# Kernel optimization log

Hardware: AMD Instinct MI355X
Metric: run time of the kernel (lower is better)

## Reference

```python
import jax, jax.numpy as jnp
import numpy as np

NEG_NUM = -10000.0
PRUNE_L, PRUNE_R = -3, 3  # prune_range


def setup_inputs() -> dict:
    key = jax.random.key(0)
    ks = jax.random.split(key, 8)
    B, L, D_CTX, D_Q, H = 32, 2048, 512, 1024, 256
    s = 0.02
    query = jax.random.normal(ks[0], (B, D_Q), jnp.float32)
    ctx = jax.random.normal(ks[1], (B, L, D_CTX), jnp.float32)
    # previous kappa (attention centre) spread over the source positions
    kappa_prev = jax.random.uniform(ks[2], (B, 1), jnp.float32) * L
    Wq = jax.random.normal(ks[3], (D_Q, H), jnp.float32) * s
    bq = jnp.zeros((H,), jnp.float32)
    Ws = jax.random.normal(ks[4], (H, 3), jnp.float32) * s
    # bias init: alpha_bias=0, beta_bias=-1, kappa_bias=-1
    bs = jnp.array([0.0, -1.0, -1.0], jnp.float32)
    W1 = jax.random.normal(ks[5], (D_CTX + D_Q, H), jnp.float32) * s
    b1 = jnp.zeros((H,), jnp.float32)
    W2 = jax.random.normal(ks[6], (H, 1), jnp.float32) * s
    b2 = jnp.zeros((1,), jnp.float32)
    return dict(query=query, ctx=ctx, kappa_prev=kappa_prev, Wq=Wq, bq=bq,
                Ws=Ws, bs=bs, W1=W1, b1=b1, W2=W2, b2=b2)


def reference(query, ctx, kappa_prev, Wq, bq, Ws, bs, W1, b1, W2, b2):
    B, L, D_CTX = ctx.shape
    # stat projection: alpha/beta/kappa (n_mixtures = 1)
    h = jnp.tanh(query @ Wq + bq)                       # [B, H]
    stat = h @ Ws + bs                                  # [B, 3]
    alpha = jnp.exp(stat[:, 0:1])                       # [B, 1]
    beta = jnp.exp(stat[:, 1:2])                        # [B, 1]
    kappa = jnp.exp(stat[:, 2:3]) + kappa_prev          # monotonic: [B, 1]

    pos = jnp.arange(L, dtype=jnp.float32)              # [L]
    diff = pos[None, :] - kappa                         # [B, L]
    prior = alpha * jnp.exp(-beta * diff * diff)        # [B, L]

    # local prune window around round(kappa) (mask built on detached kappa)
    center = jnp.round(jax.lax.stop_gradient(kappa))    # [B, 1]
    mask = (pos[None, :] >= center + PRUNE_L) & (pos[None, :] <= center + PRUNE_R)
    prior = jnp.where(mask, prior, 0.0)                 # [B, L]

    # MLP likelihood scorer over (ctx, query)
    q_exp = jnp.broadcast_to(query[:, None, :], (B, L, query.shape[1]))
    comb = jnp.concatenate([ctx, q_exp], axis=-1)       # [B, L, D_CTX+D_Q]
    score = (jnp.tanh(comb @ W1 + b1) @ W2 + b2)[..., 0]  # [B, L]
    score = jnp.where(mask, score, NEG_NUM)
    likelihood = jnp.exp(score)                         # [B, L]

    posterior = jnp.where(mask, likelihood * prior, 0.0)  # [B, L]
    p_ctx = posterior / jnp.sum(posterior, axis=-1, keepdims=True)  # normalize_post
    expected_ctx = jnp.einsum('bl,bld->bd', p_ctx, ctx)  # [B, D_CTX]
    return expected_ctx, p_ctx
```

## Files before the change

kernel.cpp:

```cpp
#include <hip/hip_runtime.h>
#include <cmath>

constexpr int B     = 32;
constexpr int L     = 2048;
constexpr int D_CTX = 512;
constexpr int D_Q   = 1024;
constexpr int H     = 256;
constexpr int PRUNE_L = -3;
constexpr int PRUNE_R = 3;
constexpr int W = PRUNE_R - PRUNE_L + 1;
constexpr int KC = 16;

__global__ __launch_bounds__(256) void partial_kernel(
    const float* __restrict__ query,
    const float* __restrict__ Wq,
    const float* __restrict__ W1,
    float* __restrict__ partQ,
    float* __restrict__ part1)
{
    const int kc = blockIdx.x;
    const int b  = blockIdx.y;
    const int j  = threadIdx.x;
    const int k0 = kc * (D_Q / KC);

    __shared__ float q_sh[D_Q / KC];
    if (j < D_Q / KC) q_sh[j] = query[b * D_Q + k0 + j];
    __syncthreads();

    const float* WqR = Wq + (size_t)k0 * H + j;
    const float* W1R = W1 + ((size_t)D_CTX + k0) * H + j;
    float accQ = 0.f, acc1 = 0.f;
#pragma unroll 16
    for (int k = 0; k < D_Q / KC; ++k) {
        const float qk = q_sh[k];
        accQ += qk * WqR[(size_t)k * H];
        acc1 += qk * W1R[(size_t)k * H];
    }
    partQ[((size_t)b * KC + kc) * H + j] = accQ;
    part1[((size_t)b * KC + kc) * H + j] = acc1;
}

__global__ __launch_bounds__(256) void stats_kernel(
    const float* __restrict__ kappa_prev,
    const float* __restrict__ bq,
    const float* __restrict__ Ws,
    const float* __restrict__ bs,
    const float* __restrict__ b1,
    const float* __restrict__ partQ,
    const float* __restrict__ part1,
    float* __restrict__ stats,
    float* __restrict__ qpre)
{
    const int b = blockIdx.x;
    const int j = threadIdx.x;

    float sq = 0.f, s1 = 0.f;
#pragma unroll
    for (int kc = 0; kc < KC; ++kc) {
        sq += partQ[((size_t)b * KC + kc) * H + j];
        s1 += part1[((size_t)b * KC + kc) * H + j];
    }
    __shared__ float h_sh[H];
    h_sh[j] = tanhf(sq + bq[j]);
    qpre[(size_t)b * H + j] = s1 + b1[j];
    __syncthreads();

    if (j < 64) {
        float s0 = 0.f, s1r = 0.f, s2 = 0.f;
#pragma unroll
        for (int i = 0; i < 4; ++i) {
            const int   jj = j + 64 * i;
            const float hv = h_sh[jj];
            s0  += hv * Ws[jj * 3 + 0];
            s1r += hv * Ws[jj * 3 + 1];
            s2  += hv * Ws[jj * 3 + 2];
        }
        for (int off = 32; off > 0; off >>= 1) {
            s0  += __shfl_down(s0, off);
            s1r += __shfl_down(s1r, off);
            s2  += __shfl_down(s2, off);
        }
        if (j == 0) {
            const float alpha = expf(s0 + bs[0]);
            const float beta  = expf(s1r + bs[1]);
            const float kappa = expf(s2 + bs[2]) + kappa_prev[b];
            stats[b * 4 + 0] = alpha;
            stats[b * 4 + 1] = beta;
            stats[b * 4 + 2] = kappa;
            stats[b * 4 + 3] = rintf(kappa);
        }
    }
}

__global__ __launch_bounds__(512) void score_kernel(
    const float* __restrict__ ctx,
    const float* __restrict__ W1,
    const float* __restrict__ W2,
    const float* __restrict__ b2,
    const float* __restrict__ stats,
    const float* __restrict__ qpre,
    float* __restrict__ post)
{
    const int t   = blockIdx.x;
    const int b   = blockIdx.y;
    const int tid = threadIdx.x;
    const int jg  = tid & 63;
    const int kc  = tid >> 6;

    const float alpha  = stats[b * 4 + 0];
    const float beta   = stats[b * 4 + 1];
    const float kappa  = stats[b * 4 + 2];
    const int   center = (int)stats[b * 4 + 3];
    const int   l      = center + PRUNE_L + t;

    if (l < 0 || l >= L) {
        if (tid == 0) post[b * W + t] = 0.0f;
        return;
    }

    __shared__ float  c_sh[D_CTX];
    __shared__ float4 part[8][64];
    __shared__ float  red[H];

    const float4* ctx4 = (const float4*)(ctx + ((size_t)b * L + (size_t)l) * D_CTX);
    if (tid < D_CTX / 4) ((float4*)c_sh)[tid] = ctx4[tid];
    __syncthreads();

    const float4* Wv = (const float4*)W1;
    float4 acc = make_float4(0.f, 0.f, 0.f, 0.f);
    const int k0 = kc * 64;
#pragma unroll 8
    for (int k = k0; k < k0 + 64; ++k) {
        const float  ck = c_sh[k];
        const float4 w  = Wv[k * 64 + jg];
        acc.x += ck * w.x; acc.y += ck * w.y;
        acc.z += ck * w.z; acc.w += ck * w.w;
    }
    part[kc][jg] = acc;
    __syncthreads();
    for (int s = 4; s > 0; s >>= 1) {
        if (kc < s) {
            float4 a = part[kc][jg], c = part[kc + s][jg];
            a.x += c.x; a.y += c.y; a.z += c.z; a.w += c.w;
            part[kc][jg] = a;
        }
        __syncthreads();
    }
    if (tid < H) {
        const float pre = ((const float*)part)[tid] + qpre[(size_t)b * H + tid];
        red[tid] = tanhf(pre) * W2[tid];
    }
    __syncthreads();
    for (int s = H / 2; s > 0; s >>= 1) {
        if (tid < s) red[tid] += red[tid + s];
        __syncthreads();
    }
    if (tid == 0) {
        const float score = red[0] + b2[0];
        const float diff  = (float)l - kappa;
        post[b * W + t] = expf(score) * alpha * expf(-beta * diff * diff);
    }
}

__global__ __launch_bounds__(256) void combine_kernel(
    const float* __restrict__ ctx,
    const float* __restrict__ stats,
    const float* __restrict__ post,
    float* __restrict__ out_e,
    float* __restrict__ out_p)
{
    const int b = blockIdx.x;
    const int j = threadIdx.x;

    __shared__ float p_sh[W];
    __shared__ int   l_sh[W];
    if (j == 0) {
        const int center = (int)stats[b * 4 + 3];
        float sum = 0.0f;
        for (int t = 0; t < W; ++t) sum += post[b * W + t];
        const float inv = 1.0f / sum;
        for (int t = 0; t < W; ++t) {
            p_sh[t] = post[b * W + t] * inv;
            l_sh[t] = center + PRUNE_L + t;
        }
    }
    __syncthreads();

    float4* prow = (float4*)(out_p + (size_t)b * L);
    const float4 z = make_float4(0.f, 0.f, 0.f, 0.f);
    prow[j]       = z;
    prow[j + 256] = z;
    __syncthreads();
    if (j < W) {
        const int l = l_sh[j];
        if (l >= 0 && l < L) out_p[(size_t)b * L + l] = p_sh[j];
    }

    if (j < D_CTX / 4) {
        float4 acc = make_float4(0.f, 0.f, 0.f, 0.f);
#pragma unroll
        for (int t = 0; t < W; ++t) {
            const int l = l_sh[t];
            if (l >= 0 && l < L) {
                const float4 c = ((const float4*)(ctx + ((size_t)b * L + (size_t)l) * D_CTX))[j];
                const float  p = p_sh[t];
                acc.x += p * c.x; acc.y += p * c.y;
                acc.z += p * c.z; acc.w += p * c.w;
            }
        }
        ((float4*)(out_e + (size_t)b * D_CTX))[j] = acc;
    }
}

extern "C" void kernel_launch(void* const* d_in, const int* in_sizes, int n_in,
                              void* d_out, int out_size, void* d_ws, size_t ws_size,
                              hipStream_t stream) {
    const float* query      = (const float*)d_in[0];
    const float* ctx        = (const float*)d_in[1];
    const float* kappa_prev = (const float*)d_in[2];
    const float* Wq         = (const float*)d_in[3];
    const float* bq         = (const float*)d_in[4];
    const float* Ws         = (const float*)d_in[5];
    const float* bs         = (const float*)d_in[6];
    const float* W1         = (const float*)d_in[7];
    const float* b1         = (const float*)d_in[8];
    const float* W2         = (const float*)d_in[9];
    const float* b2         = (const float*)d_in[10];

    float* out   = (float*)d_out;
    float* out_e = out;
    float* out_p = out + B * D_CTX;

    float* stats = (float*)d_ws;
    float* qpre  = stats + B * 4;
    float* post  = qpre + B * H;
    float* partQ = post + B * W + 8;
    float* part1 = partQ + B * KC * H;

    partial_kernel<<<dim3(KC, B), 256, 0, stream>>>(query, Wq, W1, partQ, part1);
    stats_kernel<<<B, 256, 0, stream>>>(kappa_prev, bq, Ws, bs, b1,
                                        partQ, part1, stats, qpre);
    score_kernel<<<dim3(W, B), 512, 0, stream>>>(ctx, W1, W2, b2, stats, qpre, post);
    combine_kernel<<<B, 256, 0, stream>>>(ctx, stats, post, out_e, out_p);
}
```

Baseline: 198.5 us.

## Fuse stats into score kernel, prefetch W1 rows, vectorize partial GEMV, split combine

Removes the separate stats kernel: each score block now recomputes the partial-sum reduction, tanh, the Ws projection and alpha/beta/kappa itself. Before those values are ready, it prefetches the first 16 W1 rows into registers to hide their load latency. The partial kernel now uses float4 weight loads with a 4-way k split reduced in shared memory, and the score tail uses a warp shuffle reduction instead of the shared-memory tree. Combine is spread over 8 blocks per batch row for zeroing out_p. The cost is redundant stats work across the 7 window blocks per batch and higher register pressure from the prefetched weights.

New measurement: 199.3 us. No clear change (+0.4%).

```diff
diff --git a/kernel.cpp b/kernel.cpp
--- a/kernel.cpp
+++ b/kernel.cpp
@@ -18,99 +18,121 @@
     float* __restrict__ partQ,
     float* __restrict__ part1)
 {
-    const int kc = blockIdx.x;
-    const int b  = blockIdx.y;
-    const int j  = threadIdx.x;
-    const int k0 = kc * (D_Q / KC);
-
-    __shared__ float q_sh[D_Q / KC];
-    if (j < D_Q / KC) q_sh[j] = query[b * D_Q + k0 + j];
-    __syncthreads();
-
-    const float* WqR = Wq + (size_t)k0 * H + j;
-    const float* W1R = W1 + ((size_t)D_CTX + k0) * H + j;
-    float accQ = 0.f, acc1 = 0.f;
-#pragma unroll 16
-    for (int k = 0; k < D_Q / KC; ++k) {
-        const float qk = q_sh[k];
-        accQ += qk * WqR[(size_t)k * H];
-        acc1 += qk * W1R[(size_t)k * H];
-    }
-    partQ[((size_t)b * KC + kc) * H + j] = accQ;
-    part1[((size_t)b * KC + kc) * H + j] = acc1;
-}
-
-__global__ __launch_bounds__(256) void stats_kernel(
+    const int kc  = blockIdx.x;
+    const int b   = blockIdx.y;
+    const int tid = threadIdx.x;
+    const int jg  = tid & 63;
+    const int sub = tid >> 6;
+
+    __shared__ float q_sh[64];
+    if (tid < 64) q_sh[tid] = query[b * D_Q + kc * 64 + tid];
+    __syncthreads();
+
+    const float4* WqV = (const float4*)Wq;
+    const float4* W1V = (const float4*)(W1 + (size_t)D_CTX * H);
+    float4 aQ = make_float4(0.f, 0.f, 0.f, 0.f);
+    float4 a1 = make_float4(0.f, 0.f, 0.f, 0.f);
+    const int kbase = kc * 64 + sub * 16;
+#pragma unroll
+    for (int kk = 0; kk < 16; ++kk) {
+        const int    k  = kbase + kk;
+        const float  qk = q_sh[sub * 16 + kk];
+        const float4 wq = WqV[(size_t)k * 64 + jg];
+        const float4 w1 = W1V[(size_t)k * 64 + jg];
+        aQ.x += qk * wq.x; aQ.y += qk * wq.y; aQ.z += qk * wq.z; aQ.w += qk * wq.w;
+        a1.x += qk * w1.x; a1.y += qk * w1.y; a1.z += qk * w1.z; a1.w += qk * w1.w;
+    }
+
+    __shared__ float4 pq[4][64];
+    __shared__ float4 p1[4][64];
+    pq[sub][jg] = aQ;
+    p1[sub][jg] = a1;
+    __syncthreads();
+
+    const float* pqf = (const float*)pq;
+    const float* p1f = (const float*)p1;
+    const float sQ = pqf[tid] + pqf[256 + tid] + pqf[512 + tid] + pqf[768 + tid];
+    const float s1 = p1f[tid] + p1f[256 + tid] + p1f[512 + tid] + p1f[768 + tid];
+    partQ[((size_t)b * KC + kc) * H + tid] = sQ;
+    part1[((size_t)b * KC + kc) * H + tid] = s1;
+}
+
+__global__ __launch_bounds__(512) void score_kernel(
+    const float* __restrict__ ctx,
     const float* __restrict__ kappa_prev,
     const float* __restrict__ bq,
     const float* __restrict__ Ws,
     const float* __restrict__ bs,
     const float* __restrict__ b1,
+    const float* __restrict__ W1,
+    const float* __restrict__ W2,
+    const float* __restrict__ b2,
     const float* __restrict__ partQ,
     const float* __restrict__ part1,
     float* __restrict__ stats,
-    float* __restrict__ qpre)
-{
-    const int b = blockIdx.x;
-    const int j = threadIdx.x;
-
-    float sq = 0.f, s1 = 0.f;
-#pragma unroll
-    for (int kc = 0; kc < KC; ++kc) {
-        sq += partQ[((size_t)b * KC + kc) * H + j];
-        s1 += part1[((size_t)b * KC + kc) * H + j];
-    }
-    __shared__ float h_sh[H];
-    h_sh[j] = tanhf(sq + bq[j]);
-    qpre[(size_t)b * H + j] = s1 + b1[j];
-    __syncthreads();
-
-    if (j < 64) {
-        float s0 = 0.f, s1r = 0.f, s2 = 0.f;
-#pragma unroll
-        for (int i = 0; i < 4; ++i) {
-            const int   jj = j + 64 * i;
-            const float hv = h_sh[jj];
-            s0  += hv * Ws[jj * 3 + 0];
-            s1r += hv * Ws[jj * 3 + 1];
-            s2  += hv * Ws[jj * 3 + 2];
-        }
-        for (int off = 32; off > 0; off >>= 1) {
-            s0  += __shfl_down(s0, off);
-            s1r += __shfl_down(s1r, off);
-            s2  += __shfl_down(s2, off);
-        }
-        if (j == 0) {
-            const float alpha = expf(s0 + bs[0]);
-            const float beta  = expf(s1r + bs[1]);
-            const float kappa = expf(s2 + bs[2]) + kappa_prev[b];
-            stats[b * 4 + 0] = alpha;
-            stats[b * 4 + 1] = beta;
-            stats[b * 4 + 2] = kappa;
-            stats[b * 4 + 3] = rintf(kappa);
-        }
-    }
-}
-
-__global__ __launch_bounds__(512) void score_kernel(
-    const float* __restrict__ ctx,
-    const float* __restrict__ W1,
-    const float* __restrict__ W2,
-    const float* __restrict__ b2,
-    const float* __restrict__ stats,
-    const float* __restrict__ qpre,
     float* __restrict__ post)
 {
     const int t   = blockIdx.x;
     const int b   = blockIdx.y;
     const int tid = threadIdx.x;
     const int jg  = tid & 63;
-    const int kc  = tid >> 6;
-
-    const float alpha  = stats[b * 4 + 0];
-    const float beta   = stats[b * 4 + 1];
-    const float kappa  = stats[b * 4 + 2];
-    const int   center = (int)stats[b * 4 + 3];
+    const int kc8 = tid >> 6;
+    const int k0  = kc8 * 64;
+
+    const float4* Wv = (const float4*)W1;
+    float4 wpre[16];
+#pragma unroll
+    for (int i = 0; i < 16; ++i) wpre[i] = Wv[(size_t)(k0 + i) * 64 + jg];
+
+    __shared__ float qpre_sh[H];
+    __shared__ float h_sh[H];
+    __shared__ float s_sh[4];
+    if (tid < H) {
+        float s = 0.f;
+#pragma unroll
+        for (int kc = 0; kc < KC; ++kc) s += part1[((size_t)b * KC + kc) * H + tid];
+        qpre_sh[tid] = s + b1[tid];
+    } else {
+        const int j = tid - H;
+        float s = 0.f;
+#pragma unroll
+        for (int kc = 0; kc < KC; ++kc) s += partQ[((size_t)b * KC + kc) * H + j];
+        h_sh[j] = tanhf(s + bq[j]);
+    }
+    __syncthreads();
+
+    if (tid < 64) {
+        float s0 = 0.f, s1 = 0.f, s2 = 0.f;
+#pragma unroll
+        for (int i = 0; i < 4; ++i) {
+            const int   j  = tid + 64 * i;
+            const float hv = h_sh[j];
+            s0 += hv * Ws[j * 3 + 0];
+            s1 += hv * Ws[j * 3 + 1];
+            s2 += hv * Ws[j * 3 + 2];
+        }
+        for (int off = 32; off > 0; off >>= 1) {
+            s0 += __shfl_down(s0, off);
+            s1 += __shfl_down(s1, off);
+            s2 += __shfl_down(s2, off);
+        }
+        if (tid == 0) {
+            const float alpha  = expf(s0 + bs[0]);
+            const float beta   = expf(s1 + bs[1]);
+            const float kappa  = expf(s2 + bs[2]) + kappa_prev[b];
+            const float center = rintf(kappa);
+            s_sh[0] = alpha; s_sh[1] = beta; s_sh[2] = kappa; s_sh[3] = center;
+            stats[b * 4 + 0] = alpha;
+            stats[b * 4 + 1] = beta;
+            stats[b * 4 + 2] = kappa;
+            stats[b * 4 + 3] = center;
+        }
+    }
+    __syncthreads();
+    const float alpha  = s_sh[0];
+    const float beta   = s_sh[1];
+    const float kappa  = s_sh[2];
+    const int   center = (int)s_sh[3];
     const int   l      = center + PRUNE_L + t;
 
     if (l < 0 || l >= L) {
@@ -126,39 +148,43 @@
     if (tid < D_CTX / 4) ((float4*)c_sh)[tid] = ctx4[tid];
     __syncthreads();
 
-    const float4* Wv = (const float4*)W1;
     float4 acc = make_float4(0.f, 0.f, 0.f, 0.f);
-    const int k0 = kc * 64;
-#pragma unroll 8
-    for (int k = k0; k < k0 + 64; ++k) {
-        const float  ck = c_sh[k];
-        const float4 w  = Wv[k * 64 + jg];
+#pragma unroll
+    for (int i = 0; i < 16; ++i) {
+        const float  ck = c_sh[k0 + i];
+        const float4 w  = wpre[i];
         acc.x += ck * w.x; acc.y += ck * w.y;
         acc.z += ck * w.z; acc.w += ck * w.w;
     }
-    part[kc][jg] = acc;
+#pragma unroll 8
+    for (int k = k0 + 16; k < k0 + 64; ++k) {
+        const float  ck = c_sh[k];
+        const float4 w  = Wv[(size_t)k * 64 + jg];
+        acc.x += ck * w.x; acc.y += ck * w.y;
+        acc.z += ck * w.z; acc.w += ck * w.w;
+    }
+    part[kc8][jg] = acc;
     __syncthreads();
     for (int s = 4; s > 0; s >>= 1) {
-        if (kc < s) {
-            float4 a = part[kc][jg], c = part[kc + s][jg];
+        if (kc8 < s) {
+            float4 a = part[kc8][jg], c = part[kc8 + s][jg];
             a.x += c.x; a.y += c.y; a.z += c.z; a.w += c.w;
-            part[kc][jg] = a;
+            part[kc8][jg] = a;
         }
         __syncthreads();
     }
     if (tid < H) {
-        const float pre = ((const float*)part)[tid] + qpre[(size_t)b * H + tid];
+        const float pre = ((const float*)part)[tid] + qpre_sh[tid];
         red[tid] = tanhf(pre) * W2[tid];
     }
     __syncthreads();
-    for (int s = H / 2; s > 0; s >>= 1) {
-        if (tid < s) red[tid] += red[tid + s];
-        __syncthreads();
-    }
-    if (tid == 0) {
-        const float score = red[0] + b2[0];
-        const float diff  = (float)l - kappa;
-        post[b * W + t] = expf(score) * alpha * expf(-beta * diff * diff);
+    if (tid < 64) {
+        float s = red[tid] + red[tid + 64] + red[tid + 128] + red[tid + 192];
+        for (int off = 32; off > 0; off >>= 1) s += __shfl_down(s, off);
+        if (tid == 0) {
+            const float diff = (float)l - kappa;
+            post[b * W + t] = expf(s + b2[0]) * alpha * expf(-beta * diff * diff);
+        }
     }
 }
 
@@ -169,12 +195,13 @@
     float* __restrict__ out_e,
     float* __restrict__ out_p)
 {
-    const int b = blockIdx.x;
-    const int j = threadIdx.x;
+    const int seg = blockIdx.x;
+    const int b   = blockIdx.y;
+    const int tid = threadIdx.x;
 
     __shared__ float p_sh[W];
     __shared__ int   l_sh[W];
-    if (j == 0) {
+    if (tid == 0) {
         const int center = (int)stats[b * 4 + 3];
         float sum = 0.0f;
         for (int t = 0; t < W; ++t) sum += post[b * W + t];
@@ -187,28 +214,27 @@
     __syncthreads();
 
     float4* prow = (float4*)(out_p + (size_t)b * L);
-    const float4 z = make_float4(0.f, 0.f, 0.f, 0.f);
-    prow[j]       = z;
-    prow[j + 256] = z;
-    __syncthreads();
-    if (j < W) {
-        const int l = l_sh[j];
-        if (l >= 0 && l < L) out_p[(size_t)b * L + l] = p_sh[j];
-    }
-
-    if (j < D_CTX / 4) {
+    if (tid < 64) prow[seg * 64 + tid] = make_float4(0.f, 0.f, 0.f, 0.f);
+    __syncthreads();
+    if (tid < W) {
+        const int l = l_sh[tid];
+        if (l >= seg * 256 && l < (seg + 1) * 256)
+            out_p[(size_t)b * L + l] = p_sh[tid];
+    }
+
+    if (seg == 0 && tid < D_CTX / 4) {
         float4 acc = make_float4(0.f, 0.f, 0.f, 0.f);
 #pragma unroll
         for (int t = 0; t < W; ++t) {
             const int l = l_sh[t];
             if (l >= 0 && l < L) {
-                const float4 c = ((const float4*)(ctx + ((size_t)b * L + (size_t)l) * D_CTX))[j];
+                const float4 c = ((const float4*)(ctx + ((size_t)b * L + (size_t)l) * D_CTX))[tid];
                 const float  p = p_sh[t];
                 acc.x += p * c.x; acc.y += p * c.y;
                 acc.z += p * c.z; acc.w += p * c.w;
             }
         }
-        ((float4*)(out_e + (size_t)b * D_CTX))[j] = acc;
+        ((float4*)(out_e + (size_t)b * D_CTX))[tid] = acc;
     }
 }
 
@@ -232,14 +258,12 @@
     float* out_p = out + B * D_CTX;
 
     float* stats = (float*)d_ws;
-    float* qpre  = stats + B * 4;
-    float* post  = qpre + B * H;
-    float* partQ = post + B * W + 8;
-    float* part1 = partQ + B * KC * H;
+    float* post  = stats + B * 4;
+    float* partQ = post + B * W;
+    float* part1 = partQ + (size_t)B * KC * H;
 
     partial_kernel<<<dim3(KC, B), 256, 0, stream>>>(query, Wq, W1, partQ, part1);
-    stats_kernel<<<B, 256, 0, stream>>>(kappa_prev, bq, Ws, bs, b1,
-                                        partQ, part1, stats, qpre);
-    score_kernel<<<dim3(W, B), 512, 0, stream>>>(ctx, W1, W2, b2, stats, qpre, post);
-    combine_kernel<<<B, 256, 0, stream>>>(ctx, stats, post, out_e, out_p);
-}
+    score_kernel<<<dim3(W, B), 512, 0, stream>>>(ctx, kappa_prev, bq, Ws, bs, b1,
+                                                 W1, W2, b2, partQ, part1, stats, post);
+    combine_kernel<<<dim3(8, B), 256, 0, stream>>>(ctx, stats, post, out_e, out_p);
+}
```
